# Optimization experiments

Measured on AMD Instinct MI355X. Metric: run time of the kernel, lower is better.

## Reference

```python
import jax, jax.numpy as jnp
import numpy as np

NUM_EXPERTS = 8
HIDDEN = 1024
FFN = 2048
TOKENS = 2048


def setup_inputs() -> dict:
    key = jax.random.key(0)
    k_x, k_idx, k_w1, k_w2 = jax.random.split(key, 4)
    scale = 0.02
    x = jax.random.normal(k_x, (TOKENS, HIDDEN), dtype=jnp.float32)
    expert_indices = jax.random.randint(k_idx, (TOKENS,), 0, NUM_EXPERTS, dtype=jnp.int64)
    W1 = jax.random.normal(k_w1, (NUM_EXPERTS, HIDDEN, FFN), dtype=jnp.float32) * scale
    b1 = jnp.zeros((NUM_EXPERTS, FFN), dtype=jnp.float32)
    W2 = jax.random.normal(k_w2, (NUM_EXPERTS, FFN, HIDDEN), dtype=jnp.float32) * scale
    b2 = jnp.zeros((NUM_EXPERTS, HIDDEN), dtype=jnp.float32)
    return {"x": x, "expert_indices": expert_indices, "W1": W1, "b1": b1, "W2": W2, "b2": b2}


def reference(x, expert_indices, W1, b1, W2, b2):
    # Each token routed to one expert's MLP: Linear -> GELU(exact) -> Linear.
    # Dropout is identity in eval mode. Loop is over the small fixed expert set.
    out = jnp.zeros_like(x)
    for e in range(NUM_EXPERTS):
        h = jax.nn.gelu(x @ W1[e] + b1[e], approximate=False)  # [T, FFN]
        y = h @ W2[e] + b2[e]                                   # [T, H]
        mask = (expert_indices == e)[:, None]
        out = out + jnp.where(mask, y, 0.0)
    return out
```

## Files before the change

### kernel.cpp

```cpp
#include <hip/hip_runtime.h>

#define T_TOK 2048
#define HID   1024
#define FFN   2048
#define NEXP  8
#define MAX_SLOTS 40

typedef __attribute__((ext_vector_type(8))) short bf16x8;
typedef __attribute__((ext_vector_type(4))) float f32x4;

__device__ __forceinline__ short f2bf(float f) {
    unsigned u = __builtin_bit_cast(unsigned, f);
    u = (u + 0x7fffu + ((u >> 16) & 1u)) >> 16;
    return (short)u;
}

__device__ __forceinline__ float gelu_exact(float x) {
    return 0.5f * x * (1.0f + erff(x * 0.70710678118654752f));
}

__device__ __forceinline__ void async_cp16(const short* g, short* l) {
    __builtin_amdgcn_global_load_lds(
        (const __attribute__((address_space(1))) unsigned int*)g,
        (__attribute__((address_space(3))) unsigned int*)l, 16, 0, 0);
}

__device__ __forceinline__ void wtrans_body(
        const float* __restrict__ W, short* __restrict__ WT,
        int K, int N, int e, int kblk, int nblk) {
    int tid = threadIdx.x;
    int w = tid >> 6, l = tid & 63;
    int kb = kblk * 32 + w * 8;
    int n4 = nblk * 256 + l * 4;
    const float* src = W + (size_t)e * K * N + (size_t)kb * N + n4;
    float4 v[8];
#pragma unroll
    for (int r = 0; r < 8; r++)
        v[r] = *(const float4*)(src + (size_t)r * N);
    int kpanel = kb >> 6;
    int kc = (kb >> 3) & 7;
    int npanel = n4 >> 7;
    int n_in = n4 & 127;
    int kpanels = K >> 6;
    short* dst = WT + (size_t)e * K * N
               + ((size_t)npanel * kpanels + kpanel) * 8192
               + kc * 1024 + n_in * 8;
#pragma unroll
    for (int j = 0; j < 4; j++) {
        bf16x8 o = {f2bf(((const float*)&v[0])[j]), f2bf(((const float*)&v[1])[j]),
                    f2bf(((const float*)&v[2])[j]), f2bf(((const float*)&v[3])[j]),
                    f2bf(((const float*)&v[4])[j]), f2bf(((const float*)&v[5])[j]),
                    f2bf(((const float*)&v[6])[j]), f2bf(((const float*)&v[7])[j])};
        *(bf16x8*)(dst + j * 8) = o;
    }
}

__global__ __launch_bounds__(256) void prep_kernel(
        const float* __restrict__ x, const int* __restrict__ idx,
        const float* __restrict__ b2,
        const float* __restrict__ W1, const float* __restrict__ W2,
        short* __restrict__ xb, float* __restrict__ out,
        short* __restrict__ W1T, short* __restrict__ W2T,
        int* __restrict__ offs, int* __restrict__ cnts,
        int* __restrict__ tokl,
        int* __restrict__ slot_e, int* __restrict__ slot_t0) {
    int bx = blockIdx.x;
    int tid = threadIdx.x;
    if (bx < 2048) {
        int e = bx >> 8, rem = bx & 255;
        wtrans_body(W1, W1T, HID, FFN, e, rem & 31, rem >> 5);
    } else if (bx < 4096) {
        int b = bx - 2048;
        int e = b >> 8, rem = b & 255;
        wtrans_body(W2, W2T, FFN, HID, e, rem & 63, rem >> 6);
    } else if (bx < 5120) {
        int i = ((bx - 4096) * 256 + tid) * 8;
        float4 v0 = *(const float4*)(x + i);
        float4 v1 = *(const float4*)(x + i + 4);
        bf16x8 r = {f2bf(v0.x), f2bf(v0.y), f2bf(v0.z), f2bf(v0.w),
                    f2bf(v1.x), f2bf(v1.y), f2bf(v1.z), f2bf(v1.w)};
        *(bf16x8*)(xb + i) = r;
    } else if (bx < 7168) {
        int t = bx - 5120;
        int e = idx[t];
        ((float4*)(out + (size_t)t * HID))[tid] =
            ((const float4*)(b2 + (size_t)e * HID))[tid];
    } else {
        __shared__ int c[NEXP], cur[NEXP], o[NEXP];
        if (tid < NEXP) { c[tid] = 0; cur[tid] = 0; }
        __syncthreads();
        for (int t = tid; t < T_TOK; t += 256) atomicAdd(&c[idx[t]], 1);
        __syncthreads();
        if (tid == 0) {
            int s = 0;
            for (int e = 0; e < NEXP; e++) { o[e] = s; s += c[e]; }
            int ns = 0;
            for (int e = 0; e < NEXP; e++)
                for (int t0 = 0; t0 < c[e]; t0 += 64) {
                    slot_e[ns] = e; slot_t0[ns] = t0; ns++;
                }
            for (; ns < MAX_SLOTS; ns++) slot_e[ns] = -1;
        }
        __syncthreads();
        if (tid < NEXP) { offs[tid] = o[tid]; cnts[tid] = c[tid]; }
        for (int t = tid; t < T_TOK; t += 256) {
            int e = idx[t];
            int p = o[e] + atomicAdd(&cur[e], 1);
            tokl[p] = t;
        }
    }
}

__global__ __launch_bounds__(256) void gemm1_kernel(
        const short* __restrict__ xb, const short* __restrict__ W1T,
        const float* __restrict__ b1,
        const int* __restrict__ offs, const int* __restrict__ cnts,
        const int* __restrict__ tokl,
        const int* __restrict__ slot_e, const int* __restrict__ slot_t0,
        short* __restrict__ hg) {
    int s = blockIdx.y;
    int e = slot_e[s];
    if (e < 0) return;
    int t0 = slot_t0[s], count = cnts[e], off = offs[e];
    int n0 = blockIdx.x * 128;

    __shared__ short As[64 * 64];
    __shared__ short Bs[8 * 128 * 8];
    __shared__ int stok[64];

    int tid = threadIdx.x;
    if (tid < 64) {
        int p = t0 + tid;
        stok[tid] = tokl[off + (p < count ? p : count - 1)];
    }
    __syncthreads();

    int w = tid >> 6, l = tid & 63, l15 = l & 15, quad = l >> 4;
    int wm = (w >> 1) * 32, wn = (w & 1) * 64;

    int m0 = w * 16 + (l >> 3), m1 = m0 + 8;
    int cs = l & 7;
    int c0 = (cs - m0) & 7, c1 = (cs - m1) & 7;
    const short* gA0 = xb + (size_t)stok[m0] * HID + c0 * 8;
    const short* gA1 = xb + (size_t)stok[m1] * HID + c1 * 8;
    short* lA0 = As + w * 1024 + l * 8;
    short* lA1 = lA0 + 512;

    const short* Bpan = W1T + (size_t)e * (FFN * HID)
                      + (size_t)(n0 >> 7) * ((HID >> 6) * 8192);
    int bo0 = (2 * w) * 1024 + l * 8;
    int bo1 = bo0 + 1024;
    int bo2 = bo0 + 512;
    int bo3 = bo1 + 512;

    f32x4 acc[2][4];
#pragma unroll
    for (int i = 0; i < 2; i++)
#pragma unroll
        for (int j = 0; j < 4; j++) acc[i][j] = (f32x4){0.f, 0.f, 0.f, 0.f};

    for (int kt = 0; kt < HID / 64; kt++) {
        const short* bp = Bpan + kt * 8192;
        async_cp16(gA0, lA0);
        async_cp16(gA1, lA1);
        async_cp16(bp + bo0, Bs + bo0);
        async_cp16(bp + bo1, Bs + bo1);
        async_cp16(bp + bo2, Bs + bo2);
        async_cp16(bp + bo3, Bs + bo3);
        gA0 += 64; gA1 += 64;
        __syncthreads();
        bf16x8 a[2][2], b[2][4];
#pragma unroll
        for (int kk = 0; kk < 2; kk++) {
#pragma unroll
            for (int mt = 0; mt < 2; mt++) {
                int m = wm + mt * 16 + l15;
                a[kk][mt] = *(const bf16x8*)&As[m * 64 + (((kk * 4 + quad) + m) & 7) * 8];
            }
#pragma unroll
            for (int nt = 0; nt < 4; nt++) {
                int n = wn + nt * 16 + l15;
                b[kk][nt] = *(const bf16x8*)&Bs[(kk * 4 + quad) * 1024 + n * 8];
            }
        }
#pragma unroll
        for (int kk = 0; kk < 2; kk++)
#pragma unroll
            for (int mt = 0; mt < 2; mt++)
#pragma unroll
                for (int nt = 0; nt < 4; nt++)
                    acc[mt][nt] = __builtin_amdgcn_mfma_f32_16x16x32_bf16(
                        a[kk][mt], b[kk][nt], acc[mt][nt], 0, 0, 0);
        __syncthreads();
    }

    const float* b1e = b1 + e * FFN + n0;
#pragma unroll
    for (int mt = 0; mt < 2; mt++) {
        int rbase = wm + mt * 16 + quad * 4;
#pragma unroll
        for (int nt = 0; nt < 4; nt++) {
            int coln = wn + nt * 16 + l15;
            float bb = b1e[coln];
#pragma unroll
            for (int r = 0; r < 4; r++) {
                int p = t0 + rbase + r;
                if (p < count)
                    hg[(size_t)(off + p) * FFN + n0 + coln] =
                        f2bf(gelu_exact(acc[mt][nt][r] + bb));
            }
        }
    }
}

__global__ __launch_bounds__(256) void gemm2_kernel(
        const short* __restrict__ hg, const short* __restrict__ W2T,
        const int* __restrict__ offs, const int* __restrict__ cnts,
        const int* __restrict__ tokl,
        const int* __restrict__ slot_e, const int* __restrict__ slot_t0,
        float* __restrict__ out) {
    int s = blockIdx.y;
    int e = slot_e[s];
    if (e < 0) return;
    int t0 = slot_t0[s], count = cnts[e], off = offs[e];
    int ks = blockIdx.z;
    int n0 = blockIdx.x * 128;

    __shared__ short As[64 * 64];
    __shared__ short Bs[8 * 128 * 8];

    int tid = threadIdx.x;
    int w = tid >> 6, l = tid & 63, l15 = l & 15, quad = l >> 4;
    int wm = (w >> 1) * 32, wn = (w & 1) * 64;

    int m0 = w * 16 + (l >> 3), m1 = m0 + 8;
    int cs = l & 7;
    int c0 = (cs - m0) & 7, c1 = (cs - m1) & 7;
    int g0 = off + (t0 + m0 < count ? t0 + m0 : count - 1);
    int g1 = off + (t0 + m1 < count ? t0 + m1 : count - 1);
    const short* gA0 = hg + (size_t)g0 * FFN + ks * 1024 + c0 * 8;
    const short* gA1 = hg + (size_t)g1 * FFN + ks * 1024 + c1 * 8;
    short* lA0 = As + w * 1024 + l * 8;
    short* lA1 = lA0 + 512;

    const short* Bpan = W2T + (size_t)e * (FFN * HID)
                      + (size_t)(n0 >> 7) * ((FFN >> 6) * 8192)
                      + (size_t)ks * 16 * 8192;
    int bo0 = (2 * w) * 1024 + l * 8;
    int bo1 = bo0 + 1024;
    int bo2 = bo0 + 512;
    int bo3 = bo1 + 512;

    f32x4 acc[2][4];
#pragma unroll
    for (int i = 0; i < 2; i++)
#pragma unroll
        for (int j = 0; j < 4; j++) acc[i][j] = (f32x4){0.f, 0.f, 0.f, 0.f};

    for (int kt = 0; kt < 16; kt++) {
        const short* bp = Bpan + kt * 8192;
        async_cp16(gA0, lA0);
        async_cp16(gA1, lA1);
        async_cp16(bp + bo0, Bs + bo0);
        async_cp16(bp + bo1, Bs + bo1);
        async_cp16(bp + bo2, Bs + bo2);
        async_cp16(bp + bo3, Bs + bo3);
        gA0 += 64; gA1 += 64;
        __syncthreads();
        bf16x8 a[2][2], b[2][4];
#pragma unroll
        for (int kk = 0; kk < 2; kk++) {
#pragma unroll
            for (int mt = 0; mt < 2; mt++) {
                int m = wm + mt * 16 + l15;
                a[kk][mt] = *(const bf16x8*)&As[m * 64 + (((kk * 4 + quad) + m) & 7) * 8];
            }
#pragma unroll
            for (int nt = 0; nt < 4; nt++) {
                int n = wn + nt * 16 + l15;
                b[kk][nt] = *(const bf16x8*)&Bs[(kk * 4 + quad) * 1024 + n * 8];
            }
        }
#pragma unroll
        for (int kk = 0; kk < 2; kk++)
#pragma unroll
            for (int mt = 0; mt < 2; mt++)
#pragma unroll
                for (int nt = 0; nt < 4; nt++)
                    acc[mt][nt] = __builtin_amdgcn_mfma_f32_16x16x32_bf16(
                        a[kk][mt], b[kk][nt], acc[mt][nt], 0, 0, 0);
        __syncthreads();
    }

#pragma unroll
    for (int mt = 0; mt < 2; mt++) {
        int rbase = wm + mt * 16 + quad * 4;
#pragma unroll
        for (int nt = 0; nt < 4; nt++) {
            int coln = n0 + wn + nt * 16 + l15;
#pragma unroll
            for (int r = 0; r < 4; r++) {
                int p = t0 + rbase + r;
                if (p < count) {
                    int tok = tokl[off + p];
                    atomicAdd(out + (size_t)tok * HID + coln, acc[mt][nt][r]);
                }
            }
        }
    }
}

extern "C" void kernel_launch(void* const* d_in, const int* in_sizes, int n_in,
                              void* d_out, int out_size, void* d_ws, size_t ws_size,
                              hipStream_t stream) {
    const float* x   = (const float*)d_in[0];
    const int*   idx = (const int*)d_in[1];
    const float* W1  = (const float*)d_in[2];
    const float* b1  = (const float*)d_in[3];
    const float* W2  = (const float*)d_in[4];
    const float* b2  = (const float*)d_in[5];
    float* out = (float*)d_out;

    const size_t META = 32768;
    int*   offs    = (int*)d_ws;
    int*   cnts    = offs + 8;
    int*   tokl    = offs + 16;
    int*   slot_e  = offs + 16 + T_TOK;
    int*   slot_t0 = slot_e + MAX_SLOTS;
    char*  base    = (char*)d_ws + META;
    short* xb  = (short*)base;
    short* hg  = (short*)(base + (size_t)T_TOK * HID * 2);
    short* W1T = (short*)(base + (size_t)T_TOK * HID * 2 + (size_t)T_TOK * FFN * 2);
    short* W2T = W1T + (size_t)NEXP * FFN * HID;

    prep_kernel<<<7169, 256, 0, stream>>>(
        x, idx, b2, W1, W2, xb, out, W1T, W2T,
        offs, cnts, tokl, slot_e, slot_t0);

    gemm1_kernel<<<dim3(FFN / 128, MAX_SLOTS), 256, 0, stream>>>(
        xb, W1T, b1, offs, cnts, tokl, slot_e, slot_t0, hg);
    gemm2_kernel<<<dim3(HID / 128, MAX_SLOTS, 2), 256, 0, stream>>>(
        hg, W2T, offs, cnts, tokl, slot_e, slot_t0, out);
}
```

Before: 224.5 us.

## Use 128-row token tiles and drop split-K atomics in second GEMM

Grows the per-block M tile from 64 to 128 tokens in both grouped GEMMs, so each wave computes a 64x64 sub-tile with a 4x4 MFMA accumulator. Each loaded weight panel is now reused across twice as many tokens. The second GEMM no longer splits K across two blocks; it runs the full FFN reduction and writes output plus bias directly instead of using atomicAdd. That removes the bias-initialisation pass from the prep kernel. In exchange there are far fewer blocks (at most 24 slots × 16 or 8 columns), which risks underfilling the GPU's CUs, and more accumulator registers are needed per thread.

```diff
diff --git a/kernel.cpp b/kernel.cpp
--- a/kernel.cpp
+++ b/kernel.cpp
@@ -4,7 +4,7 @@
 #define HID   1024
 #define FFN   2048
 #define NEXP  8
-#define MAX_SLOTS 40
+#define MAX_SLOTS 24
 
 typedef __attribute__((ext_vector_type(8))) short bf16x8;
 typedef __attribute__((ext_vector_type(4))) float f32x4;
@@ -57,9 +57,8 @@
 
 __global__ __launch_bounds__(256) void prep_kernel(
         const float* __restrict__ x, const int* __restrict__ idx,
-        const float* __restrict__ b2,
         const float* __restrict__ W1, const float* __restrict__ W2,
-        short* __restrict__ xb, float* __restrict__ out,
+        short* __restrict__ xb,
         short* __restrict__ W1T, short* __restrict__ W2T,
         int* __restrict__ offs, int* __restrict__ cnts,
         int* __restrict__ tokl,
@@ -80,11 +79,6 @@
         bf16x8 r = {f2bf(v0.x), f2bf(v0.y), f2bf(v0.z), f2bf(v0.w),
                     f2bf(v1.x), f2bf(v1.y), f2bf(v1.z), f2bf(v1.w)};
         *(bf16x8*)(xb + i) = r;
-    } else if (bx < 7168) {
-        int t = bx - 5120;
-        int e = idx[t];
-        ((float4*)(out + (size_t)t * HID))[tid] =
-            ((const float4*)(b2 + (size_t)e * HID))[tid];
     } else {
         __shared__ int c[NEXP], cur[NEXP], o[NEXP];
         if (tid < NEXP) { c[tid] = 0; cur[tid] = 0; }
@@ -96,7 +90,7 @@
             for (int e = 0; e < NEXP; e++) { o[e] = s; s += c[e]; }
             int ns = 0;
             for (int e = 0; e < NEXP; e++)
-                for (int t0 = 0; t0 < c[e]; t0 += 64) {
+                for (int t0 = 0; t0 < c[e]; t0 += 128) {
                     slot_e[ns] = e; slot_t0[ns] = t0; ns++;
                 }
             for (; ns < MAX_SLOTS; ns++) slot_e[ns] = -1;
@@ -124,79 +118,78 @@
     int t0 = slot_t0[s], count = cnts[e], off = offs[e];
     int n0 = blockIdx.x * 128;
 
-    __shared__ short As[64 * 64];
+    __shared__ short As[128 * 64];
     __shared__ short Bs[8 * 128 * 8];
-    __shared__ int stok[64];
+    __shared__ int stok[128];
 
     int tid = threadIdx.x;
-    if (tid < 64) {
+    if (tid < 128) {
         int p = t0 + tid;
         stok[tid] = tokl[off + (p < count ? p : count - 1)];
     }
     __syncthreads();
 
     int w = tid >> 6, l = tid & 63, l15 = l & 15, quad = l >> 4;
-    int wm = (w >> 1) * 32, wn = (w & 1) * 64;
-
-    int m0 = w * 16 + (l >> 3), m1 = m0 + 8;
-    int cs = l & 7;
-    int c0 = (cs - m0) & 7, c1 = (cs - m1) & 7;
-    const short* gA0 = xb + (size_t)stok[m0] * HID + c0 * 8;
-    const short* gA1 = xb + (size_t)stok[m1] * HID + c1 * 8;
-    short* lA0 = As + w * 1024 + l * 8;
-    short* lA1 = lA0 + 512;
-
-    const short* Bpan = W1T + (size_t)e * (FFN * HID)
+    int wm = (w >> 1) * 64, wn = (w & 1) * 64;
+    int lsub = l >> 3, cs = l & 7;
+
+    const short* gA[4];
+    short* lA[4];
+#pragma unroll
+    for (int i = 0; i < 4; i++) {
+        int m = w * 32 + i * 8 + lsub;
+        int c = (cs - m) & 7;
+        gA[i] = xb + (size_t)stok[m] * HID + c * 8;
+        lA[i] = As + w * 2048 + i * 512 + l * 8;
+    }
+
+    const short* Bpan = W1T + (size_t)e * (HID * FFN)
                       + (size_t)(n0 >> 7) * ((HID >> 6) * 8192);
-    int bo0 = (2 * w) * 1024 + l * 8;
-    int bo1 = bo0 + 1024;
-    int bo2 = bo0 + 512;
-    int bo3 = bo1 + 512;
-
-    f32x4 acc[2][4];
-#pragma unroll
-    for (int i = 0; i < 2; i++)
+    int bo[4];
+#pragma unroll
+    for (int i = 0; i < 4; i++) bo[i] = (w * 4 + i) * 512 + l * 8;
+
+    f32x4 acc[4][4];
+#pragma unroll
+    for (int i = 0; i < 4; i++)
 #pragma unroll
         for (int j = 0; j < 4; j++) acc[i][j] = (f32x4){0.f, 0.f, 0.f, 0.f};
 
     for (int kt = 0; kt < HID / 64; kt++) {
-        const short* bp = Bpan + kt * 8192;
-        async_cp16(gA0, lA0);
-        async_cp16(gA1, lA1);
-        async_cp16(bp + bo0, Bs + bo0);
-        async_cp16(bp + bo1, Bs + bo1);
-        async_cp16(bp + bo2, Bs + bo2);
-        async_cp16(bp + bo3, Bs + bo3);
-        gA0 += 64; gA1 += 64;
-        __syncthreads();
-        bf16x8 a[2][2], b[2][4];
+        const short* bp = Bpan + (size_t)kt * 8192;
+#pragma unroll
+        for (int i = 0; i < 4; i++) async_cp16(gA[i], lA[i]);
+#pragma unroll
+        for (int i = 0; i < 4; i++) async_cp16(bp + bo[i], Bs + bo[i]);
+#pragma unroll
+        for (int i = 0; i < 4; i++) gA[i] += 64;
+        __syncthreads();
 #pragma unroll
         for (int kk = 0; kk < 2; kk++) {
-#pragma unroll
-            for (int mt = 0; mt < 2; mt++) {
+            bf16x8 a[4], b[4];
+#pragma unroll
+            for (int mt = 0; mt < 4; mt++) {
                 int m = wm + mt * 16 + l15;
-                a[kk][mt] = *(const bf16x8*)&As[m * 64 + (((kk * 4 + quad) + m) & 7) * 8];
+                a[mt] = *(const bf16x8*)&As[m * 64 + (((kk * 4 + quad) + m) & 7) * 8];
             }
 #pragma unroll
             for (int nt = 0; nt < 4; nt++) {
                 int n = wn + nt * 16 + l15;
-                b[kk][nt] = *(const bf16x8*)&Bs[(kk * 4 + quad) * 1024 + n * 8];
-            }
-        }
-#pragma unroll
-        for (int kk = 0; kk < 2; kk++)
-#pragma unroll
-            for (int mt = 0; mt < 2; mt++)
+                b[nt] = *(const bf16x8*)&Bs[(kk * 4 + quad) * 1024 + n * 8];
+            }
+#pragma unroll
+            for (int mt = 0; mt < 4; mt++)
 #pragma unroll
                 for (int nt = 0; nt < 4; nt++)
                     acc[mt][nt] = __builtin_amdgcn_mfma_f32_16x16x32_bf16(
-                        a[kk][mt], b[kk][nt], acc[mt][nt], 0, 0, 0);
+                        a[mt], b[nt], acc[mt][nt], 0, 0, 0);
+        }
         __syncthreads();
     }
 
     const float* b1e = b1 + e * FFN + n0;
 #pragma unroll
-    for (int mt = 0; mt < 2; mt++) {
+    for (int mt = 0; mt < 4; mt++) {
         int rbase = wm + mt * 16 + quad * 4;
 #pragma unroll
         for (int nt = 0; nt < 4; nt++) {
@@ -215,6 +208,7 @@
 
 __global__ __launch_bounds__(256) void gemm2_kernel(
         const short* __restrict__ hg, const short* __restrict__ W2T,
+        const float* __restrict__ b2,
         const int* __restrict__ offs, const int* __restrict__ cnts,
         const int* __restrict__ tokl,
         const int* __restrict__ slot_e, const int* __restrict__ slot_t0,
@@ -223,87 +217,92 @@
     int e = slot_e[s];
     if (e < 0) return;
     int t0 = slot_t0[s], count = cnts[e], off = offs[e];
-    int ks = blockIdx.z;
     int n0 = blockIdx.x * 128;
 
-    __shared__ short As[64 * 64];
+    __shared__ short As[128 * 64];
     __shared__ short Bs[8 * 128 * 8];
+    __shared__ int stok[128];
 
     int tid = threadIdx.x;
+    if (tid < 128) {
+        int p = t0 + tid;
+        stok[tid] = tokl[off + (p < count ? p : count - 1)];
+    }
+    __syncthreads();
+
     int w = tid >> 6, l = tid & 63, l15 = l & 15, quad = l >> 4;
-    int wm = (w >> 1) * 32, wn = (w & 1) * 64;
-
-    int m0 = w * 16 + (l >> 3), m1 = m0 + 8;
-    int cs = l & 7;
-    int c0 = (cs - m0) & 7, c1 = (cs - m1) & 7;
-    int g0 = off + (t0 + m0 < count ? t0 + m0 : count - 1);
-    int g1 = off + (t0 + m1 < count ? t0 + m1 : count - 1);
-    const short* gA0 = hg + (size_t)g0 * FFN + ks * 1024 + c0 * 8;
-    const short* gA1 = hg + (size_t)g1 * FFN + ks * 1024 + c1 * 8;
-    short* lA0 = As + w * 1024 + l * 8;
-    short* lA1 = lA0 + 512;
+    int wm = (w >> 1) * 64, wn = (w & 1) * 64;
+    int lsub = l >> 3, cs = l & 7;
+
+    const short* gA[4];
+    short* lA[4];
+#pragma unroll
+    for (int i = 0; i < 4; i++) {
+        int m = w * 32 + i * 8 + lsub;
+        int c = (cs - m) & 7;
+        int gm = off + (t0 + m < count ? t0 + m : count - 1);
+        gA[i] = hg + (size_t)gm * FFN + c * 8;
+        lA[i] = As + w * 2048 + i * 512 + l * 8;
+    }
 
     const short* Bpan = W2T + (size_t)e * (FFN * HID)
-                      + (size_t)(n0 >> 7) * ((FFN >> 6) * 8192)
-                      + (size_t)ks * 16 * 8192;
-    int bo0 = (2 * w) * 1024 + l * 8;
-    int bo1 = bo0 + 1024;
-    int bo2 = bo0 + 512;
-    int bo3 = bo1 + 512;
-
-    f32x4 acc[2][4];
-#pragma unroll
-    for (int i = 0; i < 2; i++)
+                      + (size_t)(n0 >> 7) * ((FFN >> 6) * 8192);
+    int bo[4];
+#pragma unroll
+    for (int i = 0; i < 4; i++) bo[i] = (w * 4 + i) * 512 + l * 8;
+
+    f32x4 acc[4][4];
+#pragma unroll
+    for (int i = 0; i < 4; i++)
 #pragma unroll
         for (int j = 0; j < 4; j++) acc[i][j] = (f32x4){0.f, 0.f, 0.f, 0.f};
 
-    for (int kt = 0; kt < 16; kt++) {
-        const short* bp = Bpan + kt * 8192;
-        async_cp16(gA0, lA0);
-        async_cp16(gA1, lA1);
-        async_cp16(bp + bo0, Bs + bo0);
-        async_cp16(bp + bo1, Bs + bo1);
-        async_cp16(bp + bo2, Bs + bo2);
-        async_cp16(bp + bo3, Bs + bo3);
-        gA0 += 64; gA1 += 64;
-        __syncthreads();
-        bf16x8 a[2][2], b[2][4];
+    for (int kt = 0; kt < FFN / 64; kt++) {
+        const short* bp = Bpan + (size_t)kt * 8192;
+#pragma unroll
+        for (int i = 0; i < 4; i++) async_cp16(gA[i], lA[i]);
+#pragma unroll
+        for (int i = 0; i < 4; i++) async_cp16(bp + bo[i], Bs + bo[i]);
+#pragma unroll
+        for (int i = 0; i < 4; i++) gA[i] += 64;
+        __syncthreads();
 #pragma unroll
         for (int kk = 0; kk < 2; kk++) {
-#pragma unroll
-            for (int mt = 0; mt < 2; mt++) {
+            bf16x8 a[4], b[4];
+#pragma unroll
+            for (int mt = 0; mt < 4; mt++) {
                 int m = wm + mt * 16 + l15;
-                a[kk][mt] = *(const bf16x8*)&As[m * 64 + (((kk * 4 + quad) + m) & 7) * 8];
+                a[mt] = *(const bf16x8*)&As[m * 64 + (((kk * 4 + quad) + m) & 7) * 8];
             }
 #pragma unroll
             for (int nt = 0; nt < 4; nt++) {
                 int n = wn + nt * 16 + l15;
-                b[kk][nt] = *(const bf16x8*)&Bs[(kk * 4 + quad) * 1024 + n * 8];
-            }
-        }
-#pragma unroll
-        for (int kk = 0; kk < 2; kk++)
-#pragma unroll
-            for (int mt = 0; mt < 2; mt++)
+                b[nt] = *(const bf16x8*)&Bs[(kk * 4 + quad) * 1024 + n * 8];
+            }
+#pragma unroll
+            for (int mt = 0; mt < 4; mt++)
 #pragma unroll
                 for (int nt = 0; nt < 4; nt++)
                     acc[mt][nt] = __builtin_amdgcn_mfma_f32_16x16x32_bf16(
-                        a[kk][mt], b[kk][nt], acc[mt][nt], 0, 0, 0);
-        __syncthreads();
-    }
-
-#pragma unroll
-    for (int mt = 0; mt < 2; mt++) {
+                        a[mt], b[nt], acc[mt][nt], 0, 0, 0);
+        }
+        __syncthreads();
+    }
+
+    const float* b2e = b2 + e * HID + n0;
+#pragma unroll
+    for (int mt = 0; mt < 4; mt++) {
         int rbase = wm + mt * 16 + quad * 4;
 #pragma unroll
         for (int nt = 0; nt < 4; nt++) {
-            int coln = n0 + wn + nt * 16 + l15;
+            int coln = wn + nt * 16 + l15;
+            float bb = b2e[coln];
 #pragma unroll
             for (int r = 0; r < 4; r++) {
                 int p = t0 + rbase + r;
                 if (p < count) {
-                    int tok = tokl[off + p];
-                    atomicAdd(out + (size_t)tok * HID + coln, acc[mt][nt][r]);
+                    int tok = stok[rbase + r];
+                    out[(size_t)tok * HID + n0 + coln] = acc[mt][nt][r] + bb;
                 }
             }
         }
@@ -333,12 +332,12 @@
     short* W1T = (short*)(base + (size_t)T_TOK * HID * 2 + (size_t)T_TOK * FFN * 2);
     short* W2T = W1T + (size_t)NEXP * FFN * HID;
 
-    prep_kernel<<<7169, 256, 0, stream>>>(
-        x, idx, b2, W1, W2, xb, out, W1T, W2T,
+    prep_kernel<<<5121, 256, 0, stream>>>(
+        x, idx, W1, W2, xb, W1T, W2T,
         offs, cnts, tokl, slot_e, slot_t0);
 
     gemm1_kernel<<<dim3(FFN / 128, MAX_SLOTS), 256, 0, stream>>>(
         xb, W1T, b1, offs, cnts, tokl, slot_e, slot_t0, hg);
-    gemm2_kernel<<<dim3(HID / 128, MAX_SLOTS, 2), 256, 0, stream>>>(
-        hg, W2T, offs, cnts, tokl, slot_e, slot_t0, out);
-}
+    gemm2_kernel<<<dim3(HID / 128, MAX_SLOTS), 256, 0, stream>>>(
+        hg, W2T, b2, offs, cnts, tokl, slot_e, slot_t0, out);
+}
```

New measurement: 244.1 us. +8.7%, slower.

## Double-buffer LDS tiles in both expert GEMMs to overlap loads with MFMA

Applied to the files above, without the earlier changes.

Both GEMM kernels now keep two LDS buffers for the A and B tiles. Each iteration issues async global-to-LDS copies for the next k-tile before running the MFMAs on the current one, so memory latency can overlap compute instead of the loop stalling on a barrier right after each load. The gemm2 epilogue also reads token indices from a shared-memory array filled once per block, instead of reloading them from global memory for every atomic. The cost is twice the LDS per block, which may lower the number of blocks resident per CU.

```diff
diff --git a/kernel.cpp b/kernel.cpp
--- a/kernel.cpp
+++ b/kernel.cpp
@@ -124,8 +124,8 @@
     int t0 = slot_t0[s], count = cnts[e], off = offs[e];
     int n0 = blockIdx.x * 128;
 
-    __shared__ short As[64 * 64];
-    __shared__ short Bs[8 * 128 * 8];
+    __shared__ short As[2 * 64 * 64];
+    __shared__ short Bs[2 * 8 * 128 * 8];
     __shared__ int stok[64];
 
     int tid = threadIdx.x;
@@ -143,44 +143,54 @@
     int c0 = (cs - m0) & 7, c1 = (cs - m1) & 7;
     const short* gA0 = xb + (size_t)stok[m0] * HID + c0 * 8;
     const short* gA1 = xb + (size_t)stok[m1] * HID + c1 * 8;
-    short* lA0 = As + w * 1024 + l * 8;
-    short* lA1 = lA0 + 512;
-
-    const short* Bpan = W1T + (size_t)e * (FFN * HID)
+    int aoff = w * 1024 + l * 8;
+
+    const short* Bpan = W1T + (size_t)e * (HID * FFN)
                       + (size_t)(n0 >> 7) * ((HID >> 6) * 8192);
     int bo0 = (2 * w) * 1024 + l * 8;
     int bo1 = bo0 + 1024;
     int bo2 = bo0 + 512;
     int bo3 = bo1 + 512;
 
+    auto stage = [&](int buf, int kt) {
+        const short* bp = Bpan + (size_t)kt * 8192;
+        short* As_b = As + buf * 4096;
+        short* Bs_b = Bs + buf * 8192;
+        async_cp16(gA0, As_b + aoff);
+        async_cp16(gA1, As_b + aoff + 512);
+        async_cp16(bp + bo0, Bs_b + bo0);
+        async_cp16(bp + bo1, Bs_b + bo1);
+        async_cp16(bp + bo2, Bs_b + bo2);
+        async_cp16(bp + bo3, Bs_b + bo3);
+        gA0 += 64; gA1 += 64;
+    };
+
     f32x4 acc[2][4];
 #pragma unroll
     for (int i = 0; i < 2; i++)
 #pragma unroll
         for (int j = 0; j < 4; j++) acc[i][j] = (f32x4){0.f, 0.f, 0.f, 0.f};
 
-    for (int kt = 0; kt < HID / 64; kt++) {
-        const short* bp = Bpan + kt * 8192;
-        async_cp16(gA0, lA0);
-        async_cp16(gA1, lA1);
-        async_cp16(bp + bo0, Bs + bo0);
-        async_cp16(bp + bo1, Bs + bo1);
-        async_cp16(bp + bo2, Bs + bo2);
-        async_cp16(bp + bo3, Bs + bo3);
-        gA0 += 64; gA1 += 64;
-        __syncthreads();
+    stage(0, 0);
+    __syncthreads();
+
+    const int KT = HID / 64;
+    for (int kt = 0; kt < KT; kt++) {
+        if (kt + 1 < KT) stage((kt + 1) & 1, kt + 1);
+        const short* As_b = As + (kt & 1) * 4096;
+        const short* Bs_b = Bs + (kt & 1) * 8192;
         bf16x8 a[2][2], b[2][4];
 #pragma unroll
         for (int kk = 0; kk < 2; kk++) {
 #pragma unroll
             for (int mt = 0; mt < 2; mt++) {
                 int m = wm + mt * 16 + l15;
-                a[kk][mt] = *(const bf16x8*)&As[m * 64 + (((kk * 4 + quad) + m) & 7) * 8];
+                a[kk][mt] = *(const bf16x8*)&As_b[m * 64 + (((kk * 4 + quad) + m) & 7) * 8];
             }
 #pragma unroll
             for (int nt = 0; nt < 4; nt++) {
                 int n = wn + nt * 16 + l15;
-                b[kk][nt] = *(const bf16x8*)&Bs[(kk * 4 + quad) * 1024 + n * 8];
+                b[kk][nt] = *(const bf16x8*)&Bs_b[(kk * 4 + quad) * 1024 + n * 8];
             }
         }
 #pragma unroll
@@ -226,10 +236,17 @@
     int ks = blockIdx.z;
     int n0 = blockIdx.x * 128;
 
-    __shared__ short As[64 * 64];
-    __shared__ short Bs[8 * 128 * 8];
+    __shared__ short As[2 * 64 * 64];
+    __shared__ short Bs[2 * 8 * 128 * 8];
+    __shared__ int stok[64];
 
     int tid = threadIdx.x;
+    if (tid < 64) {
+        int p = t0 + tid;
+        stok[tid] = tokl[off + (p < count ? p : count - 1)];
+    }
+    __syncthreads();
+
     int w = tid >> 6, l = tid & 63, l15 = l & 15, quad = l >> 4;
     int wm = (w >> 1) * 32, wn = (w & 1) * 64;
 
@@ -240,8 +257,7 @@
     int g1 = off + (t0 + m1 < count ? t0 + m1 : count - 1);
     const short* gA0 = hg + (size_t)g0 * FFN + ks * 1024 + c0 * 8;
     const short* gA1 = hg + (size_t)g1 * FFN + ks * 1024 + c1 * 8;
-    short* lA0 = As + w * 1024 + l * 8;
-    short* lA1 = lA0 + 512;
+    int aoff = w * 1024 + l * 8;
 
     const short* Bpan = W2T + (size_t)e * (FFN * HID)
                       + (size_t)(n0 >> 7) * ((FFN >> 6) * 8192)
@@ -251,34 +267,45 @@
     int bo2 = bo0 + 512;
     int bo3 = bo1 + 512;
 
+    auto stage = [&](int buf, int kt) {
+        const short* bp = Bpan + (size_t)kt * 8192;
+        short* As_b = As + buf * 4096;
+        short* Bs_b = Bs + buf * 8192;
+        async_cp16(gA0, As_b + aoff);
+        async_cp16(gA1, As_b + aoff + 512);
+        async_cp16(bp + bo0, Bs_b + bo0);
+        async_cp16(bp + bo1, Bs_b + bo1);
+        async_cp16(bp + bo2, Bs_b + bo2);
+        async_cp16(bp + bo3, Bs_b + bo3);
+        gA0 += 64; gA1 += 64;
+    };
+
     f32x4 acc[2][4];
 #pragma unroll
     for (int i = 0; i < 2; i++)
 #pragma unroll
         for (int j = 0; j < 4; j++) acc[i][j] = (f32x4){0.f, 0.f, 0.f, 0.f};
 
-    for (int kt = 0; kt < 16; kt++) {
-        const short* bp = Bpan + kt * 8192;
-        async_cp16(gA0, lA0);
-        async_cp16(gA1, lA1);
-        async_cp16(bp + bo0, Bs + bo0);
-        async_cp16(bp + bo1, Bs + bo1);
-        async_cp16(bp + bo2, Bs + bo2);
-        async_cp16(bp + bo3, Bs + bo3);
-        gA0 += 64; gA1 += 64;
-        __syncthreads();
+    stage(0, 0);
+    __syncthreads();
+
+    const int KT = 16;
+    for (int kt = 0; kt < KT; kt++) {
+        if (kt + 1 < KT) stage((kt + 1) & 1, kt + 1);
+        const short* As_b = As + (kt & 1) * 4096;
+        const short* Bs_b = Bs + (kt & 1) * 8192;
         bf16x8 a[2][2], b[2][4];
 #pragma unroll
         for (int kk = 0; kk < 2; kk++) {
 #pragma unroll
             for (int mt = 0; mt < 2; mt++) {
                 int m = wm + mt * 16 + l15;
-                a[kk][mt] = *(const bf16x8*)&As[m * 64 + (((kk * 4 + quad) + m) & 7) * 8];
+                a[kk][mt] = *(const bf16x8*)&As_b[m * 64 + (((kk * 4 + quad) + m) & 7) * 8];
             }
 #pragma unroll
             for (int nt = 0; nt < 4; nt++) {
                 int n = wn + nt * 16 + l15;
-                b[kk][nt] = *(const bf16x8*)&Bs[(kk * 4 + quad) * 1024 + n * 8];
+                b[kk][nt] = *(const bf16x8*)&Bs_b[(kk * 4 + quad) * 1024 + n * 8];
             }
         }
 #pragma unroll
@@ -302,7 +329,7 @@
             for (int r = 0; r < 4; r++) {
                 int p = t0 + rbase + r;
                 if (p < count) {
-                    int tok = tokl[off + p];
+                    int tok = stok[rbase + r];
                     atomicAdd(out + (size_t)tok * HID + coln, acc[mt][nt][r]);
                 }
             }
```

After: 230.1 us. +2.5%, slower.

## Overlap W2 transpose/convert with first expert GEMM in one launch

Applied to the files above, without the earlier changes.

Moves the W2 fp32-to-bf16 transpose blocks out of the prep kernel and appends them to the first GEMM launch as extra blocks indexed past the GEMM tiles. The GEMM grid is flattened to 1D, with slot and N-tile decoded from the block index. The intent is to shorten the prep kernel's critical path and let the memory-bound W2 conversion run alongside compute-bound GEMM1 work. The risk is that the conversion blocks compete with GEMM blocks for bandwidth and CU slots, and that block scheduling order may not interleave them well.

```diff
diff --git a/kernel.cpp b/kernel.cpp
--- a/kernel.cpp
+++ b/kernel.cpp
@@ -55,12 +55,11 @@
     }
 }
 
-__global__ __launch_bounds__(256) void prep_kernel(
+__global__ __launch_bounds__(256) void prep1_kernel(
         const float* __restrict__ x, const int* __restrict__ idx,
-        const float* __restrict__ b2,
-        const float* __restrict__ W1, const float* __restrict__ W2,
+        const float* __restrict__ b2, const float* __restrict__ W1,
         short* __restrict__ xb, float* __restrict__ out,
-        short* __restrict__ W1T, short* __restrict__ W2T,
+        short* __restrict__ W1T,
         int* __restrict__ offs, int* __restrict__ cnts,
         int* __restrict__ tokl,
         int* __restrict__ slot_e, int* __restrict__ slot_t0) {
@@ -69,19 +68,15 @@
     if (bx < 2048) {
         int e = bx >> 8, rem = bx & 255;
         wtrans_body(W1, W1T, HID, FFN, e, rem & 31, rem >> 5);
-    } else if (bx < 4096) {
-        int b = bx - 2048;
-        int e = b >> 8, rem = b & 255;
-        wtrans_body(W2, W2T, FFN, HID, e, rem & 63, rem >> 6);
-    } else if (bx < 5120) {
-        int i = ((bx - 4096) * 256 + tid) * 8;
+    } else if (bx < 3072) {
+        int i = ((bx - 2048) * 256 + tid) * 8;
         float4 v0 = *(const float4*)(x + i);
         float4 v1 = *(const float4*)(x + i + 4);
         bf16x8 r = {f2bf(v0.x), f2bf(v0.y), f2bf(v0.z), f2bf(v0.w),
                     f2bf(v1.x), f2bf(v1.y), f2bf(v1.z), f2bf(v1.w)};
         *(bf16x8*)(xb + i) = r;
-    } else if (bx < 7168) {
-        int t = bx - 5120;
+    } else if (bx < 5120) {
+        int t = bx - 3072;
         int e = idx[t];
         ((float4*)(out + (size_t)t * HID))[tid] =
             ((const float4*)(b2 + (size_t)e * HID))[tid];
@@ -111,22 +106,31 @@
     }
 }
 
-__global__ __launch_bounds__(256) void gemm1_kernel(
+__global__ __launch_bounds__(256) void gemm1_w2_kernel(
         const short* __restrict__ xb, const short* __restrict__ W1T,
         const float* __restrict__ b1,
         const int* __restrict__ offs, const int* __restrict__ cnts,
         const int* __restrict__ tokl,
         const int* __restrict__ slot_e, const int* __restrict__ slot_t0,
-        short* __restrict__ hg) {
-    int s = blockIdx.y;
+        short* __restrict__ hg,
+        const float* __restrict__ W2, short* __restrict__ W2T) {
+    __shared__ short As[64 * 64];
+    __shared__ short Bs[8 * 128 * 8];
+    __shared__ int stok[64];
+
+    int bx = blockIdx.x;
+    if (bx >= 640) {
+        int b = bx - 640;
+        int e = b >> 8, rem = b & 255;
+        wtrans_body(W2, W2T, FFN, HID, e, rem & 63, rem >> 6);
+        return;
+    }
+
+    int s = bx >> 4;
     int e = slot_e[s];
     if (e < 0) return;
     int t0 = slot_t0[s], count = cnts[e], off = offs[e];
-    int n0 = blockIdx.x * 128;
-
-    __shared__ short As[64 * 64];
-    __shared__ short Bs[8 * 128 * 8];
-    __shared__ int stok[64];
+    int n0 = (bx & 15) * 128;
 
     int tid = threadIdx.x;
     if (tid < 64) {
@@ -333,12 +337,12 @@
     short* W1T = (short*)(base + (size_t)T_TOK * HID * 2 + (size_t)T_TOK * FFN * 2);
     short* W2T = W1T + (size_t)NEXP * FFN * HID;
 
-    prep_kernel<<<7169, 256, 0, stream>>>(
-        x, idx, b2, W1, W2, xb, out, W1T, W2T,
-        offs, cnts, tokl, slot_e, slot_t0);
-
-    gemm1_kernel<<<dim3(FFN / 128, MAX_SLOTS), 256, 0, stream>>>(
-        xb, W1T, b1, offs, cnts, tokl, slot_e, slot_t0, hg);
+    prep1_kernel<<<5121, 256, 0, stream>>>(
+        x, idx, b2, W1, xb, out, W1T, offs, cnts, tokl, slot_e, slot_t0);
+
+    gemm1_w2_kernel<<<2688, 256, 0, stream>>>(
+        xb, W1T, b1, offs, cnts, tokl, slot_e, slot_t0, hg, W2, W2T);
+
     gemm2_kernel<<<dim3(HID / 128, MAX_SLOTS, 2), 256, 0, stream>>>(
         hg, W2T, offs, cnts, tokl, slot_e, slot_t0, out);
 }
```

New measurement: 224.8 us. No clear change (+0.1%).
